# Kernel tuning notes

Hardware: AMD Instinct MI355X
Metric: run time of the kernel (lower is better)

## Reference

```python
import jax, jax.numpy as jnp
import numpy as np

B, H, N, D = 4, 16, 2048, 64

def setup_inputs() -> dict:
    key = jax.random.key(0)
    kq, kk, kv = jax.random.split(key, 3)
    q = jax.random.normal(kq, (B, H, N, D), dtype=jnp.float32)
    k = jax.random.normal(kk, (B, H, N, D), dtype=jnp.float32)
    v = jax.random.normal(kv, (B, H, N, D), dtype=jnp.float32)
    return {"q": q, "k": k, "v": v}

def reference(q, k, v):
    scale = q.shape[-1] ** -0.5
    # sim: [b, h, i, j]
    sim = jnp.einsum('bhid,bhjd->bhij', q, k) * scale
    attn = jax.nn.softmax(sim, axis=-1)  # dropout p=0.0 -> identity
    out = jnp.einsum('bhij,bhjd->bhid', attn, v)
    return out
```

## Files before the change

### kernel.cpp

```cpp
#include <hip/hip_runtime.h>
#include <stdint.h>


#define NSEQ 2048
#define DH   64
#define BHN  64
#define NIT  32

typedef short bf16x8 __attribute__((ext_vector_type(8)));
typedef float f32x4  __attribute__((ext_vector_type(4)));
typedef float f32x16 __attribute__((ext_vector_type(16)));

__device__ __forceinline__ uint16_t f2bf(float x) {
    uint32_t u = __builtin_bit_cast(uint32_t, x);
    return (uint16_t)((u + 0x7fffu + ((u >> 16) & 1u)) >> 16);
}
__device__ __forceinline__ uint32_t pk2(float a, float b) {
    return (uint32_t)f2bf(a) | ((uint32_t)f2bf(b) << 16);
}

__global__ __launch_bounds__(256) void prepass(const float* __restrict__ K,
                                               const float* __restrict__ V,
                                               uint16_t* __restrict__ F) {
    __shared__ float T0[64 * 68];
    __shared__ float T1[64 * 68];
    const int b = blockIdx.x, bh = b >> 5, kt = b & 31, t = threadIdx.x;
    const size_t gbase = ((size_t)bh * NSEQ + (size_t)kt * 64) * DH;
    const int n = t >> 2, d0 = (t & 3) * 16;
    #pragma unroll
    for (int i = 0; i < 4; ++i) {
        *(float4*)&T0[n * 68 + d0 + i * 4] = *(const float4*)(K + gbase + n * 64 + d0 + i * 4);
        *(float4*)&T1[n * 68 + d0 + i * 4] = *(const float4*)(V + gbase + n * 64 + d0 + i * 4);
    }
    __syncthreads();
    uint16_t* out = F + (size_t)(bh * 32 + kt) * 8192;
    #pragma unroll
    for (int p = 0; p < 4; ++p) {
        const int e = p * 256 + t, c = e >> 6, l = e & 63;
        const int ll = l & 31, hh = l >> 5;
        float f[8];
        if (c < 8) {
            const int row = (c >> 2) * 32 + ll;
            const int col = hh * 8 + (c & 3) * 16;
            #pragma unroll
            for (int j = 0; j < 8; ++j) f[j] = T0[row * 68 + col + j];
        } else {
            const int cc = c - 8, ktg = cc >> 1;
            const int d = (cc & 1) * 32 + ll;
            #pragma unroll
            for (int j = 0; j < 8; ++j) {
                const int i = hh * 8 + j;
                const int s = (i & 3) + 8 * ((i >> 2) & 1) + 4 * ((i >> 3) & 1);
                f[j] = T1[(ktg * 16 + s) * 68 + d];
            }
        }
        uint4 o = make_uint4(pk2(f[0], f[1]), pk2(f[2], f[3]),
                             pk2(f[4], f[5]), pk2(f[6], f[7]));
        *(uint4*)(out + (size_t)c * 512 + l * 8) = o;
    }
}

__global__ __launch_bounds__(64, 2) void attn_main(const float* __restrict__ Qg,
                                                   const uint16_t* __restrict__ F,
                                                   float* __restrict__ Og) {
    const int lane = threadIdx.x;
    const int l31 = lane & 31, h = lane >> 5;
    const int idx = blockIdx.x;
    const int bh = (idx & 7) * 8 + ((idx >> 3) & 7);
    const int qt = idx >> 6;

    const float qscale = 0.125f * 1.44269504f;
    bf16x8 qf[2][4];
    #pragma unroll
    for (int nt = 0; nt < 2; ++nt) {
        const float* qp = Qg + ((size_t)bh * NSEQ +
                                (size_t)(qt * 64 + nt * 32 + l31)) * DH + h * 8;
        #pragma unroll
        for (int k2 = 0; k2 < 4; ++k2) {
            float4 a = *(const float4*)(qp + k2 * 16);
            float4 c = *(const float4*)(qp + k2 * 16 + 4);
            union { uint32_t u[4]; bf16x8 v; } pk;
            pk.u[0] = pk2(a.x * qscale, a.y * qscale);
            pk.u[1] = pk2(a.z * qscale, a.w * qscale);
            pk.u[2] = pk2(c.x * qscale, c.y * qscale);
            pk.u[3] = pk2(c.z * qscale, c.w * qscale);
            qf[nt][k2] = pk.v;
        }
    }

    f32x16 oacc[2][2] = {};
    float lsum[2] = {0.0f, 0.0f};

    const uint16_t* fb = F + (size_t)bh * 32 * 8192 + (size_t)lane * 8;

    #pragma unroll 1
    for (int kt = 0; kt < NIT; ++kt) {
        uint4 kc[8], vc[8];
        #pragma unroll
        for (int c = 0; c < 8; ++c) kc[c] = *(const uint4*)(fb + (size_t)c * 512);
        #pragma unroll
        for (int c = 0; c < 8; ++c) vc[c] = *(const uint4*)(fb + (size_t)(8 + c) * 512);
        fb += 8192;

        #pragma unroll
        for (int mtj = 0; mtj < 2; ++mtj) {
            #pragma unroll
            for (int nt = 0; nt < 2; ++nt) {
                f32x16 s = {};
                #pragma unroll
                for (int k2 = 0; k2 < 4; ++k2)
                    s = __builtin_amdgcn_mfma_f32_32x32x16_bf16(
                        __builtin_bit_cast(bf16x8, kc[mtj * 4 + k2]), qf[nt][k2], s, 0, 0, 0);
                bf16x8 pf[2];
                float ls = 0.0f;
                #pragma unroll
                for (int ktl = 0; ktl < 2; ++ktl) {
                    union { uint32_t u[4]; bf16x8 v; } pp;
                    #pragma unroll
                    for (int t2 = 0; t2 < 4; ++t2) {
                        float e0 = __builtin_amdgcn_exp2f(s[ktl * 8 + 2 * t2]);
                        float e1 = __builtin_amdgcn_exp2f(s[ktl * 8 + 2 * t2 + 1]);
                        ls += e0 + e1;
                        pp.u[t2] = __builtin_amdgcn_perm(
                            __builtin_bit_cast(uint32_t, e1),
                            __builtin_bit_cast(uint32_t, e0), 0x07060302u);
                    }
                    pf[ktl] = pp.v;
                }
                lsum[nt] += ls;
                #pragma unroll
                for (int nd = 0; nd < 2; ++nd) {
                    oacc[nt][nd] = __builtin_amdgcn_mfma_f32_32x32x16_bf16(
                        pf[0], __builtin_bit_cast(bf16x8, vc[(2 * mtj + 0) * 2 + nd]),
                        oacc[nt][nd], 0, 0, 0);
                    oacc[nt][nd] = __builtin_amdgcn_mfma_f32_32x32x16_bf16(
                        pf[1], __builtin_bit_cast(bf16x8, vc[(2 * mtj + 1) * 2 + nd]),
                        oacc[nt][nd], 0, 0, 0);
                }
            }
        }
    }

    float* Ob = Og + (size_t)bh * NSEQ * DH;
    #pragma unroll
    for (int nt = 0; nt < 2; ++nt) {
        float lt = lsum[nt] + __shfl_xor(lsum[nt], 32);
        float rinv = 1.0f / lt;
        int rib = __builtin_bit_cast(int, rinv);
        #pragma unroll
        for (int rg = 0; rg < 16; ++rg) {
            const int il = (rg & 3) + 8 * (rg >> 2) + 4 * h;
            const float inv = __builtin_bit_cast(float,
                __builtin_amdgcn_ds_bpermute(il * 4, rib));
            const int row = qt * 64 + nt * 32 + il;
            #pragma unroll
            for (int nd = 0; nd < 2; ++nd)
                Ob[(size_t)row * DH + nd * 32 + l31] = oacc[nt][nd][rg] * inv;
        }
    }
}

#define LDS_S 72
#define NWAVE 4
#define BN    64
__global__ __launch_bounds__(256) void attn_fwd_fb(const float* __restrict__ Qg,
                                                   const float* __restrict__ Kg,
                                                   const float* __restrict__ Vg,
                                                   float* __restrict__ Og) {
    __shared__ short KsF[BN * LDS_S];
    __shared__ short VtsF[DH * LDS_S];
    __shared__ short PsF[NWAVE * 16 * LDS_S];
    const int tid = threadIdx.x;
    const int wave = tid >> 6, lane = tid & 63, quad = lane >> 4, l16 = lane & 15;
    const int bh = blockIdx.x >> 5, qtf = blockIdx.x & 31;
    const size_t base = (size_t)bh * NSEQ * DH;
    const float* Qb = Qg + base; const float* Kbf = Kg + base;
    const float* Vb = Vg + base; float* Ob = Og + base;
    const float qscale = 0.125f * 1.44269504f;
    bf16x8 qfrag[2];
    {
        const int qrow = qtf * 64 + wave * 16 + l16;
        const float* qp = Qb + (size_t)qrow * DH + quad * 8;
        #pragma unroll
        for (int c = 0; c < 2; ++c) {
            float4 x = *(const float4*)(qp + 32 * c);
            float4 y = *(const float4*)(qp + 32 * c + 4);
            union { uint16_t u[8]; bf16x8 v; } pk;
            pk.u[0]=f2bf(x.x*qscale); pk.u[1]=f2bf(x.y*qscale);
            pk.u[2]=f2bf(x.z*qscale); pk.u[3]=f2bf(x.w*qscale);
            pk.u[4]=f2bf(y.x*qscale); pk.u[5]=f2bf(y.y*qscale);
            pk.u[6]=f2bf(y.z*qscale); pk.u[7]=f2bf(y.w*qscale);
            qfrag[c] = pk.v;
        }
    }
    f32x4 o[4] = {};
    float m_i[4], l_i[4];
    #pragma unroll
    for (int r = 0; r < 4; ++r) { m_i[r] = -1e30f; l_i[r] = 0.0f; }
    const int kr0 = tid >> 4, kd0 = (tid & 15) * 4;
    const int vp = (tid & 31) * 2, vd0 = (tid >> 5) * 8;
    #pragma unroll 1
    for (int kt = 0; kt < NSEQ / BN; ++kt) {
        __syncthreads();
        {
            const float* kbase = Kbf + (size_t)kt * BN * DH;
            #pragma unroll
            for (int jj = 0; jj < 4; ++jj) {
                const int row = kr0 + jj * 16;
                float4 x = *(const float4*)(kbase + (size_t)row * DH + kd0);
                union { uint16_t u[4]; uint64_t ll; } pk;
                pk.u[0]=f2bf(x.x); pk.u[1]=f2bf(x.y); pk.u[2]=f2bf(x.z); pk.u[3]=f2bf(x.w);
                *(uint64_t*)&KsF[row * LDS_S + kd0] = pk.ll;
            }
        }
        {
            const float* v0 = Vb + (size_t)(kt * BN + vp) * DH + vd0;
            const float* v1 = v0 + DH;
            float4 a0 = *(const float4*)(v0); float4 a1 = *(const float4*)(v0 + 4);
            float4 b0 = *(const float4*)(v1); float4 b1 = *(const float4*)(v1 + 4);
            float av[8] = {a0.x,a0.y,a0.z,a0.w,a1.x,a1.y,a1.z,a1.w};
            float bv[8] = {b0.x,b0.y,b0.z,b0.w,b1.x,b1.y,b1.z,b1.w};
            #pragma unroll
            for (int i = 0; i < 8; ++i)
                *(uint32_t*)&VtsF[(vd0 + i) * LDS_S + vp] = pk2(av[i], bv[i]);
        }
        __syncthreads();
        f32x4 s[4] = {};
        #pragma unroll
        for (int c = 0; c < 2; ++c)
            #pragma unroll
            for (int n = 0; n < 4; ++n) {
                bf16x8 kfr = *(const bf16x8*)&KsF[(n * 16 + l16) * LDS_S + quad * 8 + 32 * c];
                s[n] = __builtin_amdgcn_mfma_f32_16x16x32_bf16(qfrag[c], kfr, s[n], 0, 0, 0);
            }
        float rmax[4];
        #pragma unroll
        for (int r = 0; r < 4; ++r)
            rmax[r] = fmaxf(fmaxf(s[0][r], s[1][r]), fmaxf(s[2][r], s[3][r]));
        #pragma unroll
        for (int off = 1; off < 16; off <<= 1)
            #pragma unroll
            for (int r = 0; r < 4; ++r)
                rmax[r] = fmaxf(rmax[r], __shfl_xor(rmax[r], off, 64));
        float alpha[4], rsum[4];
        #pragma unroll
        for (int r = 0; r < 4; ++r) {
            float mn = fmaxf(m_i[r], rmax[r]);
            alpha[r] = __builtin_amdgcn_exp2f(m_i[r] - mn);
            m_i[r] = mn; rsum[r] = 0.0f;
        }
        #pragma unroll
        for (int n = 0; n < 4; ++n)
            #pragma unroll
            for (int r = 0; r < 4; ++r) {
                float p = __builtin_amdgcn_exp2f(s[n][r] - m_i[r]);
                rsum[r] += p;
                PsF[(wave * 16 + quad * 4 + r) * LDS_S + n * 16 + l16] = (short)f2bf(p);
            }
        #pragma unroll
        for (int off = 1; off < 16; off <<= 1)
            #pragma unroll
            for (int r = 0; r < 4; ++r)
                rsum[r] += __shfl_xor(rsum[r], off, 64);
        #pragma unroll
        for (int r = 0; r < 4; ++r) l_i[r] = l_i[r] * alpha[r] + rsum[r];
        #pragma unroll
        for (int n = 0; n < 4; ++n)
            #pragma unroll
            for (int r = 0; r < 4; ++r) o[n][r] *= alpha[r];
        #pragma unroll
        for (int c = 0; c < 2; ++c) {
            bf16x8 pfr = *(const bf16x8*)&PsF[(wave * 16 + l16) * LDS_S + quad * 8 + 32 * c];
            #pragma unroll
            for (int n = 0; n < 4; ++n) {
                bf16x8 vfr = *(const bf16x8*)&VtsF[(n * 16 + l16) * LDS_S + quad * 8 + 32 * c];
                o[n] = __builtin_amdgcn_mfma_f32_16x16x32_bf16(pfr, vfr, o[n], 0, 0, 0);
            }
        }
    }
    float inv[4];
    #pragma unroll
    for (int r = 0; r < 4; ++r) inv[r] = 1.0f / l_i[r];
    const int orow0 = qtf * 64 + wave * 16 + quad * 4;
    #pragma unroll
    for (int n = 0; n < 4; ++n)
        #pragma unroll
        for (int r = 0; r < 4; ++r)
            Ob[(size_t)(orow0 + r) * DH + n * 16 + l16] = o[n][r] * inv[r];
}

extern "C" void kernel_launch(void* const* d_in, const int* in_sizes, int n_in,
                              void* d_out, int out_size, void* d_ws, size_t ws_size,
                              hipStream_t stream) {
    (void)in_sizes; (void)n_in; (void)out_size;
    const float* q = (const float*)d_in[0];
    const float* k = (const float*)d_in[1];
    const float* v = (const float*)d_in[2];
    float* out = (float*)d_out;
    const size_t need = (size_t)BHN * 32 * 16384;
    if (ws_size >= need) {
        uint16_t* fbuf = (uint16_t*)d_ws;
        prepass<<<dim3(BHN * 32), dim3(256), 0, stream>>>(k, v, fbuf);
        attn_main<<<dim3(2048), dim3(64), 0, stream>>>(q, fbuf, out);
    } else {
        attn_fwd_fb<<<dim3(BHN * 32), dim3(256), 0, stream>>>(q, k, v, out);
    }
}
```

Measured before the change: 196.0 us.

## Split KV range across wave pairs in 4-wave blocks with LDS reduction

The attention kernel now runs 256-thread blocks of four waves. Two wave pairs each cover 64 query rows, and within each pair the two waves take opposite halves of the key sequence. Partial output accumulators and row sums from the second half are passed through shared memory and combined before normalisation and the store. This halves the serial KV loop per wave and lets the pair share block residency, at the cost of an LDS reduction, a barrier, and half the waves sitting idle during the epilogue. The code omits max subtraction, so the two partials can be added directly.

```diff
diff --git a/kernel.cpp b/kernel.cpp
--- a/kernel.cpp
+++ b/kernel.cpp
@@ -5,7 +5,6 @@
 #define NSEQ 2048
 #define DH   64
 #define BHN  64
-#define NIT  32
 
 typedef short bf16x8 __attribute__((ext_vector_type(8)));
 typedef float f32x4  __attribute__((ext_vector_type(4)));
@@ -60,11 +59,18 @@
     }
 }
 
-__global__ __launch_bounds__(64, 2) void attn_main(const float* __restrict__ Qg,
-                                                   const uint16_t* __restrict__ F,
-                                                   float* __restrict__ Og) {
-    const int lane = threadIdx.x;
+__global__ __launch_bounds__(256, 4) void attn_main(const float* __restrict__ Qg,
+                                                    const uint16_t* __restrict__ F,
+                                                    float* __restrict__ Og) {
+    __shared__ __align__(16) float Obuf[32 * 64 * 4];
+    __shared__ float Lpart[2][64];
+
+    const int tid = threadIdx.x;
+    const int w = tid >> 6, lane = tid & 63;
     const int l31 = lane & 31, h = lane >> 5;
+    const int w01 = w & 1;
+    const int hv  = w >> 1;
+
     const int idx = blockIdx.x;
     const int bh = (idx & 7) * 8 + ((idx >> 3) & 7);
     const int qt = idx >> 6;
@@ -74,7 +80,7 @@
     #pragma unroll
     for (int nt = 0; nt < 2; ++nt) {
         const float* qp = Qg + ((size_t)bh * NSEQ +
-                                (size_t)(qt * 64 + nt * 32 + l31)) * DH + h * 8;
+                                (size_t)(qt * 128 + w01 * 64 + nt * 32 + l31)) * DH + h * 8;
         #pragma unroll
         for (int k2 = 0; k2 < 4; ++k2) {
             float4 a = *(const float4*)(qp + k2 * 16);
@@ -91,10 +97,10 @@
     f32x16 oacc[2][2] = {};
     float lsum[2] = {0.0f, 0.0f};
 
-    const uint16_t* fb = F + (size_t)bh * 32 * 8192 + (size_t)lane * 8;
+    const uint16_t* fb = F + ((size_t)bh * 32 + hv * 16) * 8192 + (size_t)lane * 8;
 
     #pragma unroll 1
-    for (int kt = 0; kt < NIT; ++kt) {
+    for (int kt = 0; kt < 16; ++kt) {
         uint4 kc[8], vc[8];
         #pragma unroll
         for (int c = 0; c < 8; ++c) kc[c] = *(const uint4*)(fb + (size_t)c * 512);
@@ -141,18 +147,51 @@
         }
     }
 
+    lsum[0] += __shfl_xor(lsum[0], 32);
+    lsum[1] += __shfl_xor(lsum[1], 32);
+
+    if (hv == 1) {
+        #pragma unroll
+        for (int nt = 0; nt < 2; ++nt)
+            #pragma unroll
+            for (int nd = 0; nd < 2; ++nd)
+                #pragma unroll
+                for (int rg4 = 0; rg4 < 4; ++rg4) {
+                    const int slot = w01 * 16 + (nt * 2 + nd) * 4 + rg4;
+                    f32x4 v;
+                    #pragma unroll
+                    for (int j = 0; j < 4; ++j) v[j] = oacc[nt][nd][rg4 * 4 + j];
+                    *(f32x4*)&Obuf[(slot * 64 + lane) * 4] = v;
+                }
+        if (h == 0) {
+            Lpart[w01][l31]      = lsum[0];
+            Lpart[w01][32 + l31] = lsum[1];
+        }
+    }
+    __syncthreads();
+    if (hv == 1) return;
+
     float* Ob = Og + (size_t)bh * NSEQ * DH;
     #pragma unroll
     for (int nt = 0; nt < 2; ++nt) {
-        float lt = lsum[nt] + __shfl_xor(lsum[nt], 32);
-        float rinv = 1.0f / lt;
-        int rib = __builtin_bit_cast(int, rinv);
+        #pragma unroll
+        for (int nd = 0; nd < 2; ++nd)
+            #pragma unroll
+            for (int rg4 = 0; rg4 < 4; ++rg4) {
+                const int slot = w01 * 16 + (nt * 2 + nd) * 4 + rg4;
+                f32x4 v = *(const f32x4*)&Obuf[(slot * 64 + lane) * 4];
+                #pragma unroll
+                for (int j = 0; j < 4; ++j) oacc[nt][nd][rg4 * 4 + j] += v[j];
+            }
+        const float lc = lsum[nt] + Lpart[w01][nt * 32 + l31];
+        const float rinv = 1.0f / lc;
+        const int rib = __builtin_bit_cast(int, rinv);
         #pragma unroll
         for (int rg = 0; rg < 16; ++rg) {
             const int il = (rg & 3) + 8 * (rg >> 2) + 4 * h;
             const float inv = __builtin_bit_cast(float,
                 __builtin_amdgcn_ds_bpermute(il * 4, rib));
-            const int row = qt * 64 + nt * 32 + il;
+            const int row = qt * 128 + w01 * 64 + nt * 32 + il;
             #pragma unroll
             for (int nd = 0; nd < 2; ++nd)
                 Ob[(size_t)row * DH + nd * 32 + l31] = oacc[nt][nd][rg] * inv;
@@ -301,7 +340,7 @@
     if (ws_size >= need) {
         uint16_t* fbuf = (uint16_t*)d_ws;
         prepass<<<dim3(BHN * 32), dim3(256), 0, stream>>>(k, v, fbuf);
-        attn_main<<<dim3(2048), dim3(64), 0, stream>>>(q, fbuf, out);
+        attn_main<<<dim3(1024), dim3(256), 0, stream>>>(q, fbuf, out);
     } else {
         attn_fwd_fb<<<dim3(BHN * 32), dim3(256), 0, stream>>>(q, k, v, out);
     }
```

Result: slower. 599.5 us (+205.9%).
